# Kernel tuning notes

Hardware: AMD Instinct MI355X
Metric: run time of the kernel (lower is better)

Reference implementation:

```python
import jax, jax.numpy as jnp
import numpy as np

B, S, D = 1, 2048, 4096
H, KV = 32, 8
HD = D // H  # 128
NEG = -1e9


def _rope(t, cos, sin):
    # t: [B,S,h,HD]; cos/sin: [S,HD//2] -> broadcast [1,S,1,HD//2]
    tr = t[..., 0::2]
    ti = t[..., 1::2]
    c = cos[None, :, None, :]
    s = sin[None, :, None, :]
    out_r = tr * c - ti * s
    out_i = tr * s + ti * c
    # interleave back: (..., HD//2, 2) -> (..., HD)
    return jnp.stack([out_r, out_i], axis=-1).reshape(t.shape)


def setup_inputs() -> dict:
    key = jax.random.key(0)
    ks = jax.random.split(key, 5)
    w_scale = 0.02
    x = jax.random.normal(ks[0], (B, S, D), dtype=jnp.float32)
    wq = jax.random.normal(ks[1], (H * HD, D), dtype=jnp.float32) * w_scale
    wk = jax.random.normal(ks[2], (KV * HD, D), dtype=jnp.float32) * w_scale
    wv = jax.random.normal(ks[3], (KV * HD, D), dtype=jnp.float32) * w_scale
    wo = jax.random.normal(ks[4], (D, H * HD), dtype=jnp.float32) * w_scale
    # RoPE tables (theta = 10000)
    inv_freq = 1.0 / (10000.0 ** (np.arange(0, HD, 2, dtype=np.float32) / HD))
    angles = np.arange(S, dtype=np.float32)[:, None] * inv_freq[None, :]  # [S, HD//2]
    freqs_cos = jnp.asarray(np.cos(angles))
    freqs_sin = jnp.asarray(np.sin(angles))
    # causal additive mask [1,1,S,S]
    causal = jnp.tril(jnp.ones((S, S), dtype=bool))
    mask = jnp.where(causal, 0.0, NEG).astype(jnp.float32)[None, None]
    return {"x": x, "wq": wq, "wk": wk, "wv": wv, "wo": wo,
            "freqs_cos": freqs_cos, "freqs_sin": freqs_sin, "mask": mask}


def reference(x, wq, wk, wv, wo, freqs_cos, freqs_sin, mask):
    b, s, d = x.shape
    q = (x @ wq.T).reshape(b, s, H, HD)
    k = (x @ wk.T).reshape(b, s, KV, HD)
    v = (x @ wv.T).reshape(b, s, KV, HD)
    q = _rope(q, freqs_cos, freqs_sin)
    k = _rope(k, freqs_cos, freqs_sin)
    rep = H // KV
    k = jnp.repeat(k, rep, axis=2)  # [b,s,H,HD]
    v = jnp.repeat(v, rep, axis=2)
    scores = jnp.einsum('bshd,bthd->bhst', q, k) / jnp.sqrt(jnp.float32(HD))
    scores = scores + mask
    attn = jax.nn.softmax(scores, axis=-1)
    out = jnp.einsum('bhst,bthd->bshd', attn, v).reshape(b, s, H * HD)
    return out @ wo.T
```

## Files before the change

### kernel.cpp

```cpp
#include <hip/hip_runtime.h>
#include <hip/hip_bf16.h>
#include <math.h>

#define SEQ 2048
#define DIM 4096
#define NH 32
#define NKV 8
#define HD 128
#define KVD 1024
#define SCALE 0.08838834764831845f
#define NEGBIG -1000000000.0f

typedef __bf16 bf16;
typedef __attribute__((ext_vector_type(2))) __bf16 bf16x2;
typedef __attribute__((ext_vector_type(4))) __bf16 bf16x4;
typedef __attribute__((ext_vector_type(8))) __bf16 bf16x8;
typedef __attribute__((ext_vector_type(4))) float f32x4;

__device__ __forceinline__ void async_g2l16(const bf16* g, bf16* l) {
  __builtin_amdgcn_global_load_lds(
      (const __attribute__((address_space(1))) void*)g,
      (__attribute__((address_space(3))) void*)l,
      16, 0, 0);
}

__global__ void cast_bf16_kernel(const float* __restrict__ in,
                                 bf16* __restrict__ out, int n4) {
  int i = blockIdx.x * 256 + threadIdx.x;
  if (i >= n4) return;
  float4 v = ((const float4*)in)[i];
  bf16x4 o;
  o[0] = (bf16)v.x; o[1] = (bf16)v.y; o[2] = (bf16)v.z; o[3] = (bf16)v.w;
  ((bf16x4*)out)[i] = o;
}

__device__ __forceinline__ void gemm_bt_body(
    const bf16* __restrict__ A, int lda,
    const bf16* __restrict__ B, int ldb,
    float* __restrict__ C, int ldc,
    int K, int mBase)
{
  __shared__ __align__(16) bf16 As[128 * 32];
  __shared__ __align__(16) bf16 Bs[128 * 32];

  const int tid  = threadIdx.x;
  const int lane = tid & 63;
  const int w    = tid >> 6;
  const int l15  = lane & 15;
  const int quad = lane >> 4;
  const int wr   = (w >> 1) * 64;
  const int wc   = (w & 1) * 64;

  const int srow = lane >> 2;
  const int skp  = (lane & 3) * 8;
  const bf16* gA0 = A + (size_t)(mBase + w * 16 + srow) * lda + skp;
  const bf16* gA1 = gA0 + (size_t)64 * lda;
  const bf16* gB0 = B + (size_t)(w * 16 + srow) * ldb + skp;
  const bf16* gB1 = gB0 + (size_t)64 * ldb;
  bf16* lA0 = As + w * 512;
  bf16* lA1 = As + (w + 4) * 512;
  bf16* lB0 = Bs + w * 512;
  bf16* lB1 = Bs + (w + 4) * 512;

  const f32x4 vzero = {0.f, 0.f, 0.f, 0.f};
  f32x4 acc[4][4];
#pragma unroll
  for (int mi = 0; mi < 4; ++mi)
#pragma unroll
    for (int ni = 0; ni < 4; ++ni) acc[mi][ni] = vzero;

  for (int k0 = 0; k0 < K; k0 += 32) {
    __syncthreads();
    async_g2l16(gA0 + k0, lA0);
    async_g2l16(gA1 + k0, lA1);
    async_g2l16(gB0 + k0, lB0);
    async_g2l16(gB1 + k0, lB1);
    __syncthreads();

    bf16x8 a[4], b[4];
#pragma unroll
    for (int mi = 0; mi < 4; ++mi)
      a[mi] = *(const bf16x8*)(As + (wr + mi * 16 + l15) * 32 + quad * 8);
#pragma unroll
    for (int ni = 0; ni < 4; ++ni)
      b[ni] = *(const bf16x8*)(Bs + (wc + ni * 16 + l15) * 32 + quad * 8);
#pragma unroll
    for (int mi = 0; mi < 4; ++mi)
#pragma unroll
      for (int ni = 0; ni < 4; ++ni)
        acc[mi][ni] = __builtin_amdgcn_mfma_f32_16x16x32_bf16(
            a[mi], b[ni], acc[mi][ni], 0, 0, 0);
  }

#pragma unroll
  for (int mi = 0; mi < 4; ++mi) {
    int row = mBase + wr + mi * 16 + quad * 4;
#pragma unroll
    for (int ni = 0; ni < 4; ++ni) {
      int col = wc + ni * 16 + l15;
#pragma unroll
      for (int r = 0; r < 4; ++r)
        C[(size_t)(row + r) * ldc + col] = acc[mi][ni][r];
    }
  }
}

__global__ __launch_bounds__(256, 2) void qkv_gemm_kernel(
    const bf16* __restrict__ xb, const bf16* __restrict__ wqb,
    const bf16* __restrict__ wkb, const bf16* __restrict__ wvb,
    float* __restrict__ Qf, float* __restrict__ Kf, float* __restrict__ Vf)
{
  int nb = blockIdx.x;
  const bf16* B; float* C; int ldc;
  if (nb < 32)      { B = wqb + (size_t)nb * 128 * DIM;        C = Qf + nb * 128;        ldc = DIM; }
  else if (nb < 40) { int t = nb - 32; B = wkb + (size_t)t * 128 * DIM; C = Kf + t * 128; ldc = KVD; }
  else              { int t = nb - 40; B = wvb + (size_t)t * 128 * DIM; C = Vf + t * 128; ldc = KVD; }
  gemm_bt_body(xb, DIM, B, DIM, C, ldc, DIM, blockIdx.y * 128);
}

__global__ __launch_bounds__(256, 2) void out_gemm_kernel(
    const bf16* __restrict__ attnb, const bf16* __restrict__ wob,
    float* __restrict__ out)
{
  gemm_bt_body(attnb, DIM, wob + (size_t)blockIdx.x * 128 * DIM, DIM,
               out + blockIdx.x * 128, DIM, DIM, blockIdx.y * 128);
}

__global__ void rope_q_kernel(const float* __restrict__ Qf,
                              const float* __restrict__ Cb,
                              const float* __restrict__ Sb,
                              bf16* __restrict__ Qb) {
  int i = blockIdx.x * 256 + threadIdx.x;
  int di = i & 63;
  int h  = (i >> 6) & (NH - 1);
  int s  = i >> 11;
  size_t base = (size_t)s * DIM + h * HD + 2 * di;
  float2 t = *(const float2*)(Qf + base);
  float c = Cb[s * 64 + di], sn = Sb[s * 64 + di];
  bf16x2 o;
  o[0] = (bf16)((t.x * c - t.y * sn) * SCALE);
  o[1] = (bf16)((t.x * sn + t.y * c) * SCALE);
  *(bf16x2*)(Qb + base) = o;
}

__global__ void rope_k_kernel(const float* __restrict__ Kf,
                              const float* __restrict__ Cb,
                              const float* __restrict__ Sb,
                              bf16* __restrict__ Kb) {
  int i = blockIdx.x * 256 + threadIdx.x;
  int di = i & 63;
  int h  = (i >> 6) & (NKV - 1);
  int s  = i >> 9;
  size_t base = (size_t)s * KVD + h * HD + 2 * di;
  float2 t = *(const float2*)(Kf + base);
  float c = Cb[s * 64 + di], sn = Sb[s * 64 + di];
  bf16x2 o;
  o[0] = (bf16)(t.x * c - t.y * sn);
  o[1] = (bf16)(t.x * sn + t.y * c);
  *(bf16x2*)(Kb + base) = o;
}

__global__ void vtrans_kernel(const float* __restrict__ Vf,
                              bf16* __restrict__ Vt) {
  __shared__ float tile[32][33];
  int kv = blockIdx.z;
  int d0 = blockIdx.y * 32, s0 = blockIdx.x * 32;
  int tx = threadIdx.x, ty = threadIdx.y;
  tile[ty][tx] = Vf[(size_t)(s0 + ty) * KVD + kv * HD + d0 + tx];
  __syncthreads();
  Vt[(size_t)kv * HD * SEQ + (size_t)(d0 + ty) * SEQ + s0 + tx] =
      (bf16)tile[tx][ty];
}

__global__ __launch_bounds__(256, 2) void attn_kernel(
    const bf16* __restrict__ Qb, const bf16* __restrict__ Kb,
    const bf16* __restrict__ Vt, bf16* __restrict__ attnb)
{
  __shared__ __align__(16) bf16 Ks[64 * 128];
  __shared__ __align__(16) bf16 Vs[128 * 64];
  __shared__ __align__(16) bf16 Ps[128 * 64];

  const int b    = blockIdx.x;
  const int half = b >> 8;
  const int r8   = b & 255;
  const int h    = (half << 4) | (r8 >> 4);
  const int qt   = half ? (r8 & 15) : 15 - (r8 & 15);
  const int kvh  = h >> 2;
  const int qbase = qt * 128;

  const int tid  = threadIdx.x;
  const int lane = tid & 63;
  const int w    = tid >> 6;
  const int l15  = lane & 15;
  const int quad = lane >> 4;

  bf16x8 qfrag[2][4];
#pragma unroll
  for (int n = 0; n < 2; ++n) {
    int q = qbase + w * 32 + n * 16 + l15;
#pragma unroll
    for (int ks = 0; ks < 4; ++ks)
      qfrag[n][ks] = *(const bf16x8*)(Qb + (size_t)q * DIM + h * HD +
                                      ks * 32 + quad * 8);
  }

  const f32x4 vzero = {0.f, 0.f, 0.f, 0.f};
  f32x4 oacc[8][2];
#pragma unroll
  for (int dm = 0; dm < 8; ++dm)
#pragma unroll
    for (int n = 0; n < 2; ++n) oacc[dm][n] = vzero;
  float m_run[2] = {-1e30f, -1e30f};
  float l_run[2] = {0.f, 0.f};

  const int nkt = 2 * (qt + 1);
  for (int kt = 0; kt < nkt; ++kt) {
    const int kbase = kt * 64;

    __syncthreads();
#pragma unroll
    for (int t = 0; t < 4; ++t) {
      int kr0 = w * 16 + t * 4;
      int krow = kr0 + (lane >> 4);
      int kg = (lane & 15) ^ (krow & 7);
      async_g2l16(Kb + (size_t)(kbase + krow) * KVD + kvh * HD + kg * 8,
                  Ks + kr0 * 128);
      int vr0 = w * 32 + t * 8;
      int d = vr0 + (lane >> 3);
      int vg = (lane & 7) ^ (d & 7);
      async_g2l16(Vt + ((size_t)kvh * HD + d) * SEQ + kbase + vg * 8,
                  Vs + vr0 * 64);
    }
    __syncthreads();

    f32x4 sacc[4][2];
#pragma unroll
    for (int kg = 0; kg < 4; ++kg)
#pragma unroll
      for (int n = 0; n < 2; ++n) sacc[kg][n] = vzero;
#pragma unroll
    for (int kg = 0; kg < 4; ++kg) {
      bf16x8 kf[4];
#pragma unroll
      for (int ks = 0; ks < 4; ++ks) {
        int row = kg * 16 + l15;
        kf[ks] = *(const bf16x8*)(Ks + row * 128 +
                                  (((ks * 4 + quad) ^ (row & 7)) * 8));
      }
#pragma unroll
      for (int n = 0; n < 2; ++n)
#pragma unroll
        for (int ks = 0; ks < 4; ++ks)
          sacc[kg][n] = __builtin_amdgcn_mfma_f32_16x16x32_bf16(
              kf[ks], qfrag[n][ks], sacc[kg][n], 0, 0, 0);
    }

#pragma unroll
    for (int n = 0; n < 2; ++n) {
      const int qloc = w * 32 + n * 16 + l15;
      const int qglob = qbase + qloc;
      if (kbase + 63 > qbase + w * 32 + n * 16) {
#pragma unroll
        for (int kg = 0; kg < 4; ++kg)
#pragma unroll
          for (int r = 0; r < 4; ++r) {
            int key = kbase + kg * 16 + quad * 4 + r;
            if (key > qglob) sacc[kg][n][r] = NEGBIG;
          }
      }
      float mx = -1e30f;
#pragma unroll
      for (int kg = 0; kg < 4; ++kg)
#pragma unroll
        for (int r = 0; r < 4; ++r) mx = fmaxf(mx, sacc[kg][n][r]);
      mx = fmaxf(mx, __shfl_xor(mx, 16, 64));
      mx = fmaxf(mx, __shfl_xor(mx, 32, 64));
      float mnew = fmaxf(m_run[n], mx);
      float alpha = __expf(m_run[n] - mnew);
      m_run[n] = mnew;
      float rs = 0.f;
#pragma unroll
      for (int kg = 0; kg < 4; ++kg) {
        bf16x4 pk;
#pragma unroll
        for (int r = 0; r < 4; ++r) {
          float p = __expf(sacc[kg][n][r] - mnew);
          rs += p;
          pk[r] = (bf16)p;
        }
        int g16 = (kg * 2 + (quad >> 1)) ^ (qloc & 7);
        *(bf16x4*)(Ps + qloc * 64 + g16 * 8 + (quad & 1) * 4) = pk;
      }
      rs += __shfl_xor(rs, 16, 64);
      rs += __shfl_xor(rs, 32, 64);
      l_run[n] = alpha * l_run[n] + rs;
#pragma unroll
      for (int dm = 0; dm < 8; ++dm)
#pragma unroll
        for (int r = 0; r < 4; ++r) oacc[dm][n][r] *= alpha;
    }

    bf16x8 pf[2][2];
#pragma unroll
    for (int kk = 0; kk < 2; ++kk)
#pragma unroll
      for (int n = 0; n < 2; ++n) {
        int qloc = w * 32 + n * 16 + l15;
        pf[kk][n] = *(const bf16x8*)(Ps + qloc * 64 +
                                     (((kk * 4 + quad) ^ (qloc & 7)) * 8));
      }
#pragma unroll
    for (int dm = 0; dm < 8; ++dm) {
#pragma unroll
      for (int kk = 0; kk < 2; ++kk) {
        int d = dm * 16 + l15;
        bf16x8 vf = *(const bf16x8*)(Vs + d * 64 +
                                     (((kk * 4 + quad) ^ (d & 7)) * 8));
#pragma unroll
        for (int n = 0; n < 2; ++n)
          oacc[dm][n] = __builtin_amdgcn_mfma_f32_16x16x32_bf16(
              vf, pf[kk][n], oacc[dm][n], 0, 0, 0);
      }
    }
  }

#pragma unroll
  for (int n = 0; n < 2; ++n) {
    float inv = 1.0f / l_run[n];
    int q = qbase + w * 32 + n * 16 + l15;
#pragma unroll
    for (int dm = 0; dm < 8; ++dm) {
      bf16x4 ov;
#pragma unroll
      for (int r = 0; r < 4; ++r) ov[r] = (bf16)(oacc[dm][n][r] * inv);
      *(bf16x4*)(attnb + (size_t)q * DIM + h * HD + dm * 16 + quad * 4) = ov;
    }
  }
}

extern "C" void kernel_launch(void* const* d_in, const int* in_sizes, int n_in,
                              void* d_out, int out_size, void* d_ws, size_t ws_size,
                              hipStream_t stream) {
  const float* x  = (const float*)d_in[0];
  const float* wq = (const float*)d_in[1];
  const float* wk = (const float*)d_in[2];
  const float* wv = (const float*)d_in[3];
  const float* wo = (const float*)d_in[4];
  const float* fc = (const float*)d_in[5];
  const float* fs = (const float*)d_in[6];
  float* out = (float*)d_out;

  size_t off = 0;
  char* wsb = (char*)d_ws;
  auto take = [&](size_t bytes) -> void* {
    void* p = wsb + off;
    off += (bytes + 255) & ~(size_t)255;
    return p;
  };
  bf16*  xb    = (bf16*)take((size_t)SEQ * DIM * 2);
  bf16*  wqb   = (bf16*)take((size_t)DIM * DIM * 2);
  bf16*  wkb   = (bf16*)take((size_t)KVD * DIM * 2);
  bf16*  wvb   = (bf16*)take((size_t)KVD * DIM * 2);
  bf16*  wob   = (bf16*)take((size_t)DIM * DIM * 2);
  float* Qf    = (float*)take((size_t)SEQ * DIM * 4);
  float* Kf    = (float*)take((size_t)SEQ * KVD * 4);
  float* Vf    = (float*)take((size_t)SEQ * KVD * 4);
  bf16*  Qb    = (bf16*)take((size_t)SEQ * DIM * 2);
  bf16*  Kb    = (bf16*)take((size_t)SEQ * KVD * 2);
  bf16*  Vt    = (bf16*)take((size_t)NKV * HD * SEQ * 2);
  bf16*  attnb = (bf16*)take((size_t)SEQ * DIM * 2);

  cast_bf16_kernel<<<(SEQ * DIM / 4) / 256, 256, 0, stream>>>(x, xb, SEQ * DIM / 4);
  cast_bf16_kernel<<<(DIM * DIM / 4) / 256, 256, 0, stream>>>(wq, wqb, DIM * DIM / 4);
  cast_bf16_kernel<<<(KVD * DIM / 4) / 256, 256, 0, stream>>>(wk, wkb, KVD * DIM / 4);
  cast_bf16_kernel<<<(KVD * DIM / 4) / 256, 256, 0, stream>>>(wv, wvb, KVD * DIM / 4);
  cast_bf16_kernel<<<(DIM * DIM / 4) / 256, 256, 0, stream>>>(wo, wob, DIM * DIM / 4);

  qkv_gemm_kernel<<<dim3(48, 16), 256, 0, stream>>>(xb, wqb, wkb, wvb, Qf, Kf, Vf);

  rope_q_kernel<<<(SEQ * NH * 64) / 256, 256, 0, stream>>>(Qf, fc, fs, Qb);
  rope_k_kernel<<<(SEQ * NKV * 64) / 256, 256, 0, stream>>>(Kf, fc, fs, Kb);
  vtrans_kernel<<<dim3(SEQ / 32, HD / 32, NKV), dim3(32, 32), 0, stream>>>(Vf, Vt);

  attn_kernel<<<dim3(512), 256, 0, stream>>>(Qb, Kb, Vt, attnb);

  out_gemm_kernel<<<dim3(32, 16), 256, 0, stream>>>(attnb, wob, out);
}
```

Before: 517.9 us.

## Fuse RoPE and V transpose into QKV GEMM epilogue, merge casts, swizzle LDS

Fuses the RoPE application for Q and K, plus the bf16 V transpose, directly into the QKV GEMM epilogue. This removes the fp32 Q/K/V intermediate buffers and three separate elementwise kernels. The five cast launches become one kernel that dispatches by index range. An XOR swizzle is added to the LDS layout of the GEMM tiles to reduce bank conflicts on fragment loads. The epilogue now does uncoalesced scalar bf16 stores and a shuffle per element, which may cost some GEMM efficiency.

```diff
diff --git a/kernel.cpp b/kernel.cpp
--- a/kernel.cpp
+++ b/kernel.cpp
@@ -24,21 +24,40 @@
       16, 0, 0);
 }
 
-__global__ void cast_bf16_kernel(const float* __restrict__ in,
-                                 bf16* __restrict__ out, int n4) {
+#define SEG_X  2097152
+#define SEG_WQ 4194304
+#define SEG_WK 1048576
+#define C0 SEG_X
+#define C1 (C0 + SEG_WQ)
+#define C2 (C1 + SEG_WK)
+#define C3 (C2 + SEG_WK)
+#define C4 (C3 + SEG_WQ)
+
+__global__ void cast_all_kernel(const float* __restrict__ x,
+                                const float* __restrict__ wq,
+                                const float* __restrict__ wk,
+                                const float* __restrict__ wv,
+                                const float* __restrict__ wo,
+                                bf16* __restrict__ xb, bf16* __restrict__ wqb,
+                                bf16* __restrict__ wkb, bf16* __restrict__ wvb,
+                                bf16* __restrict__ wob) {
   int i = blockIdx.x * 256 + threadIdx.x;
-  if (i >= n4) return;
-  float4 v = ((const float4*)in)[i];
+  const float* src; bf16* dst; int j;
+  if (i < C0)      { src = x;  dst = xb;  j = i; }
+  else if (i < C1) { src = wq; dst = wqb; j = i - C0; }
+  else if (i < C2) { src = wk; dst = wkb; j = i - C1; }
+  else if (i < C3) { src = wv; dst = wvb; j = i - C2; }
+  else             { src = wo; dst = wob; j = i - C3; }
+  float4 v = ((const float4*)src)[j];
   bf16x4 o;
   o[0] = (bf16)v.x; o[1] = (bf16)v.y; o[2] = (bf16)v.z; o[3] = (bf16)v.w;
-  ((bf16x4*)out)[i] = o;
-}
-
-__device__ __forceinline__ void gemm_bt_body(
+  ((bf16x4*)dst)[j] = o;
+}
+
+__device__ __forceinline__ void gemm_core(
     const bf16* __restrict__ A, int lda,
     const bf16* __restrict__ B, int ldb,
-    float* __restrict__ C, int ldc,
-    int K, int mBase)
+    int K, int mBase, f32x4 acc[4][4])
 {
   __shared__ __align__(16) bf16 As[128 * 32];
   __shared__ __align__(16) bf16 Bs[128 * 32];
@@ -52,10 +71,10 @@
   const int wc   = (w & 1) * 64;
 
   const int srow = lane >> 2;
-  const int skp  = (lane & 3) * 8;
-  const bf16* gA0 = A + (size_t)(mBase + w * 16 + srow) * lda + skp;
+  const int kswz = ((lane & 3) ^ ((srow >> 1) & 3)) * 8;
+  const bf16* gA0 = A + (size_t)(mBase + w * 16 + srow) * lda + kswz;
   const bf16* gA1 = gA0 + (size_t)64 * lda;
-  const bf16* gB0 = B + (size_t)(w * 16 + srow) * ldb + skp;
+  const bf16* gB0 = B + (size_t)(w * 16 + srow) * ldb + kswz;
   const bf16* gB1 = gB0 + (size_t)64 * ldb;
   bf16* lA0 = As + w * 512;
   bf16* lA1 = As + (w + 4) * 512;
@@ -63,11 +82,12 @@
   bf16* lB1 = Bs + (w + 4) * 512;
 
   const f32x4 vzero = {0.f, 0.f, 0.f, 0.f};
-  f32x4 acc[4][4];
 #pragma unroll
   for (int mi = 0; mi < 4; ++mi)
 #pragma unroll
     for (int ni = 0; ni < 4; ++ni) acc[mi][ni] = vzero;
+
+  const int rsw = ((l15 >> 1) & 3);
 
   for (int k0 = 0; k0 < K; k0 += 32) {
     __syncthreads();
@@ -80,10 +100,12 @@
     bf16x8 a[4], b[4];
 #pragma unroll
     for (int mi = 0; mi < 4; ++mi)
-      a[mi] = *(const bf16x8*)(As + (wr + mi * 16 + l15) * 32 + quad * 8);
+      a[mi] = *(const bf16x8*)(As + (wr + mi * 16 + l15) * 32 +
+                               ((quad ^ rsw) * 8));
 #pragma unroll
     for (int ni = 0; ni < 4; ++ni)
-      b[ni] = *(const bf16x8*)(Bs + (wc + ni * 16 + l15) * 32 + quad * 8);
+      b[ni] = *(const bf16x8*)(Bs + (wc + ni * 16 + l15) * 32 +
+                               ((quad ^ rsw) * 8));
 #pragma unroll
     for (int mi = 0; mi < 4; ++mi)
 #pragma unroll
@@ -91,85 +113,100 @@
         acc[mi][ni] = __builtin_amdgcn_mfma_f32_16x16x32_bf16(
             a[mi], b[ni], acc[mi][ni], 0, 0, 0);
   }
-
-#pragma unroll
-  for (int mi = 0; mi < 4; ++mi) {
-    int row = mBase + wr + mi * 16 + quad * 4;
-#pragma unroll
-    for (int ni = 0; ni < 4; ++ni) {
-      int col = wc + ni * 16 + l15;
-#pragma unroll
-      for (int r = 0; r < 4; ++r)
-        C[(size_t)(row + r) * ldc + col] = acc[mi][ni][r];
-    }
-  }
 }
 
 __global__ __launch_bounds__(256, 2) void qkv_gemm_kernel(
     const bf16* __restrict__ xb, const bf16* __restrict__ wqb,
     const bf16* __restrict__ wkb, const bf16* __restrict__ wvb,
-    float* __restrict__ Qf, float* __restrict__ Kf, float* __restrict__ Vf)
+    const float* __restrict__ fc, const float* __restrict__ fs,
+    bf16* __restrict__ Qb, bf16* __restrict__ Kb, bf16* __restrict__ Vt)
 {
-  int nb = blockIdx.x;
-  const bf16* B; float* C; int ldc;
-  if (nb < 32)      { B = wqb + (size_t)nb * 128 * DIM;        C = Qf + nb * 128;        ldc = DIM; }
-  else if (nb < 40) { int t = nb - 32; B = wkb + (size_t)t * 128 * DIM; C = Kf + t * 128; ldc = KVD; }
-  else              { int t = nb - 40; B = wvb + (size_t)t * 128 * DIM; C = Vf + t * 128; ldc = KVD; }
-  gemm_bt_body(xb, DIM, B, DIM, C, ldc, DIM, blockIdx.y * 128);
+  const int nb = blockIdx.x;
+  const int mBase = blockIdx.y * 128;
+  const bf16* Bm;
+  if (nb < 32)      Bm = wqb + (size_t)nb * 128 * DIM;
+  else if (nb < 40) Bm = wkb + (size_t)(nb - 32) * 128 * DIM;
+  else              Bm = wvb + (size_t)(nb - 40) * 128 * DIM;
+
+  f32x4 acc[4][4];
+  gemm_core(xb, DIM, Bm, DIM, DIM, mBase, acc);
+
+  const int tid  = threadIdx.x;
+  const int lane = tid & 63;
+  const int w    = tid >> 6;
+  const int l15  = lane & 15;
+  const int quad = lane >> 4;
+  const int wr   = (w >> 1) * 64;
+  const int wc   = (w & 1) * 64;
+
+  if (nb < 40) {
+    const bool isQ = (nb < 32);
+    bf16* dst = isQ ? (Qb + nb * HD) : (Kb + (nb - 32) * HD);
+    const int ldd = isQ ? DIM : KVD;
+    const float sc = isQ ? SCALE : 1.0f;
+    const int odd = l15 & 1;
+#pragma unroll
+    for (int mi = 0; mi < 4; ++mi) {
+#pragma unroll
+      for (int ni = 0; ni < 4; ++ni) {
+        int d = wc + ni * 16 + l15;
+        int fidx = d >> 1;
+#pragma unroll
+        for (int r = 0; r < 4; ++r) {
+          int s = mBase + wr + mi * 16 + quad * 4 + r;
+          float v  = acc[mi][ni][r];
+          float pv = __shfl_xor(v, 1, 64);
+          float c  = fc[s * 64 + fidx];
+          float sn = fs[s * 64 + fidx];
+          float o  = odd ? (pv * sn + v * c) : (v * c - pv * sn);
+          dst[(size_t)s * ldd + d] = (bf16)(o * sc);
+        }
+      }
+    }
+  } else {
+    const int t = nb - 40;
+#pragma unroll
+    for (int mi = 0; mi < 4; ++mi) {
+      int srow = mBase + wr + mi * 16 + quad * 4;
+#pragma unroll
+      for (int ni = 0; ni < 4; ++ni) {
+        int d = wc + ni * 16 + l15;
+        bf16x4 pv;
+#pragma unroll
+        for (int r = 0; r < 4; ++r) pv[r] = (bf16)acc[mi][ni][r];
+        *(bf16x4*)(Vt + ((size_t)t * HD + d) * SEQ + srow) = pv;
+      }
+    }
+  }
 }
 
 __global__ __launch_bounds__(256, 2) void out_gemm_kernel(
     const bf16* __restrict__ attnb, const bf16* __restrict__ wob,
     float* __restrict__ out)
 {
-  gemm_bt_body(attnb, DIM, wob + (size_t)blockIdx.x * 128 * DIM, DIM,
-               out + blockIdx.x * 128, DIM, DIM, blockIdx.y * 128);
-}
-
-__global__ void rope_q_kernel(const float* __restrict__ Qf,
-                              const float* __restrict__ Cb,
-                              const float* __restrict__ Sb,
-                              bf16* __restrict__ Qb) {
-  int i = blockIdx.x * 256 + threadIdx.x;
-  int di = i & 63;
-  int h  = (i >> 6) & (NH - 1);
-  int s  = i >> 11;
-  size_t base = (size_t)s * DIM + h * HD + 2 * di;
-  float2 t = *(const float2*)(Qf + base);
-  float c = Cb[s * 64 + di], sn = Sb[s * 64 + di];
-  bf16x2 o;
-  o[0] = (bf16)((t.x * c - t.y * sn) * SCALE);
-  o[1] = (bf16)((t.x * sn + t.y * c) * SCALE);
-  *(bf16x2*)(Qb + base) = o;
-}
-
-__global__ void rope_k_kernel(const float* __restrict__ Kf,
-                              const float* __restrict__ Cb,
-                              const float* __restrict__ Sb,
-                              bf16* __restrict__ Kb) {
-  int i = blockIdx.x * 256 + threadIdx.x;
-  int di = i & 63;
-  int h  = (i >> 6) & (NKV - 1);
-  int s  = i >> 9;
-  size_t base = (size_t)s * KVD + h * HD + 2 * di;
-  float2 t = *(const float2*)(Kf + base);
-  float c = Cb[s * 64 + di], sn = Sb[s * 64 + di];
-  bf16x2 o;
-  o[0] = (bf16)(t.x * c - t.y * sn);
-  o[1] = (bf16)(t.x * sn + t.y * c);
-  *(bf16x2*)(Kb + base) = o;
-}
-
-__global__ void vtrans_kernel(const float* __restrict__ Vf,
-                              bf16* __restrict__ Vt) {
-  __shared__ float tile[32][33];
-  int kv = blockIdx.z;
-  int d0 = blockIdx.y * 32, s0 = blockIdx.x * 32;
-  int tx = threadIdx.x, ty = threadIdx.y;
-  tile[ty][tx] = Vf[(size_t)(s0 + ty) * KVD + kv * HD + d0 + tx];
-  __syncthreads();
-  Vt[(size_t)kv * HD * SEQ + (size_t)(d0 + ty) * SEQ + s0 + tx] =
-      (bf16)tile[tx][ty];
+  const int mBase = blockIdx.y * 128;
+  f32x4 acc[4][4];
+  gemm_core(attnb, DIM, wob + (size_t)blockIdx.x * 128 * DIM, DIM, DIM,
+            mBase, acc);
+
+  const int tid  = threadIdx.x;
+  const int lane = tid & 63;
+  const int w    = tid >> 6;
+  const int l15  = lane & 15;
+  const int quad = lane >> 4;
+  const int wr   = (w >> 1) * 64;
+  const int wc   = (w & 1) * 64;
+#pragma unroll
+  for (int mi = 0; mi < 4; ++mi) {
+    int row = mBase + wr + mi * 16 + quad * 4;
+#pragma unroll
+    for (int ni = 0; ni < 4; ++ni) {
+      int col = blockIdx.x * 128 + wc + ni * 16 + l15;
+#pragma unroll
+      for (int r = 0; r < 4; ++r)
+        out[(size_t)(row + r) * DIM + col] = acc[mi][ni][r];
+    }
+  }
 }
 
 __global__ __launch_bounds__(256, 2) void attn_kernel(
@@ -362,25 +399,16 @@
   bf16*  wkb   = (bf16*)take((size_t)KVD * DIM * 2);
   bf16*  wvb   = (bf16*)take((size_t)KVD * DIM * 2);
   bf16*  wob   = (bf16*)take((size_t)DIM * DIM * 2);
-  float* Qf    = (float*)take((size_t)SEQ * DIM * 4);
-  float* Kf    = (float*)take((size_t)SEQ * KVD * 4);
-  float* Vf    = (float*)take((size_t)SEQ * KVD * 4);
   bf16*  Qb    = (bf16*)take((size_t)SEQ * DIM * 2);
   bf16*  Kb    = (bf16*)take((size_t)SEQ * KVD * 2);
   bf16*  Vt    = (bf16*)take((size_t)NKV * HD * SEQ * 2);
   bf16*  attnb = (bf16*)take((size_t)SEQ * DIM * 2);
 
-  cast_bf16_kernel<<<(SEQ * DIM / 4) / 256, 256, 0, stream>>>(x, xb, SEQ * DIM / 4);
-  cast_bf16_kernel<<<(DIM * DIM / 4) / 256, 256, 0, stream>>>(wq, wqb, DIM * DIM / 4);
-  cast_bf16_kernel<<<(KVD * DIM / 4) / 256, 256, 0, stream>>>(wk, wkb, KVD * DIM / 4);
-  cast_bf16_kernel<<<(KVD * DIM / 4) / 256, 256, 0, stream>>>(wv, wvb, KVD * DIM / 4);
-  cast_bf16_kernel<<<(DIM * DIM / 4) / 256, 256, 0, stream>>>(wo, wob, DIM * DIM / 4);
-
-  qkv_gemm_kernel<<<dim3(48, 16), 256, 0, stream>>>(xb, wqb, wkb, wvb, Qf, Kf, Vf);
-
-  rope_q_kernel<<<(SEQ * NH * 64) / 256, 256, 0, stream>>>(Qf, fc, fs, Qb);
-  rope_k_kernel<<<(SEQ * NKV * 64) / 256, 256, 0, stream>>>(Kf, fc, fs, Kb);
-  vtrans_kernel<<<dim3(SEQ / 32, HD / 32, NKV), dim3(32, 32), 0, stream>>>(Vf, Vt);
+  cast_all_kernel<<<C4 / 256, 256, 0, stream>>>(x, wq, wk, wv, wo,
+                                                xb, wqb, wkb, wvb, wob);
+
+  qkv_gemm_kernel<<<dim3(48, 16), 256, 0, stream>>>(xb, wqb, wkb, wvb,
+                                                    fc, fs, Qb, Kb, Vt);
 
   attn_kernel<<<dim3(512), 256, 0, stream>>>(Qb, Kb, Vt, attnb);
 
```

Result: faster. 483.1 us (-6.7%).
